# Kernel optimization log

Hardware: AMD Instinct MI355X
Metric: run time of the kernel (lower is better)

The kernel has to match this reference:

```python
import jax, jax.numpy as jnp
import numpy as np

K, NR, NT, D, NLAYER = 128, 1, 128, 1, 8
PMAX = float(np.power(10.0, 10.0 / 10.0))  # snr=10 dB
SIGMA = 1.0


def _cx(x):
    # [2, ...] real/imag-stacked -> complex
    return x[0] + 1j * x[1]


def _ct(x):
    # conjugate transpose on last two axes
    return jnp.conj(jnp.swapaxes(x, -1, -2))


def _layer(Vc, Hc, up1, up3, up4, wp1, wp3, vp1, vp2, vp4):
    # Vc: [K,Nt,d] complex, Hc: [K,Nr,Nt] complex; params complex, batched over K.
    cdt = Vc.dtype
    I_nr = jnp.eye(NR, dtype=cdt)
    I_d = jnp.eye(D, dtype=cdt)
    I_nt = jnp.eye(NT, dtype=cdt)
    # ---- A_update: A_i = sigma/Pmax * sum_j tr(V_j V_j^H) * I + H_i (sum_j V_j V_j^H) H_i^H
    tr_vv = jnp.einsum('knd,knd->', Vc, jnp.conj(Vc))          # complex scalar
    S = jnp.einsum('knd,kmd->nm', Vc, jnp.conj(Vc))            # [Nt,Nt]
    A = (SIGMA / PMAX) * tr_vv * I_nr + jnp.einsum('krt,tm,ksm->krs', Hc, S, jnp.conj(Hc))  # [K,Nr,Nr]
    # ---- U layer: A_inv_i = p1_i inv(A_i) + 0.01 p3_i ; U_i = A_inv_i H_i V_i + p4_i
    A_inv = up1 @ jnp.linalg.inv(A) + 0.01 * up3
    Un = A_inv @ Hc @ Vc + up4                                  # [K,Nr,d]
    # ---- E_update: E_i = I - U_i^H H_i V_i
    E = I_d - _ct(Un) @ Hc @ Vc                                 # [K,d,d]
    # ---- W layer: W_i = 0.1 p1_i inv(E_i) + 0.01 p3_i
    Wn = 0.1 * (wp1 @ jnp.linalg.inv(E)) + 0.01 * wp3           # [K,d,d]
    # ---- B_update: B = sigma/Pmax * sum_i tr(U_i W_i U_i^H) * I + sum_i H_i^H U_i W_i U_i^H H_i (same for all users)
    UWU = Un @ Wn @ _ct(Un)                                     # [K,Nr,Nr]
    tr_uwu = jnp.trace(UWU, axis1=-2, axis2=-1).sum()
    B = (SIGMA / PMAX) * tr_uwu * I_nt + jnp.sum(_ct(Hc) @ UWU @ Hc, axis=0)  # [Nt,Nt]
    B_inv = jnp.linalg.inv(B)
    # ---- V
    if vp2 is None:  # FinalV: V_i = inv(B) H_i^H U_i W_i
        Vn = (B_inv @ _ct(Hc)) @ Un @ Wn
    else:            # V layer: B_inv_i = p2_i inv(B) + 0.01 p4_i ; V_i = B_inv_i H_i^H U_i W_i + p1_i
        Bm = vp2 @ B_inv + 0.01 * vp4
        Vn = Bm @ _ct(Hc) @ Un @ Wn + vp1
    # ---- Normalize: scale by sqrt(Pmax)/sqrt(Re sum_j tr(V_j V_j^H))
    pw = jnp.sqrt(jnp.real(jnp.einsum('knd,knd->', Vn, jnp.conj(Vn))))
    return (jnp.sqrt(PMAX) / pw) * Vn


def setup_inputs() -> dict:
    key = jax.random.key(0)
    ks = jax.random.split(key, 20)
    f32 = jnp.float32
    def rn(k, shape, scale):
        return (scale * jax.random.normal(k, shape)).astype(f32)
    inp = {
        'V': rn(ks[0], (2, K, NT, D), 1.0),
        'H': rn(ks[1], (2, K, NR, NT), 1.0),
        # mid-layer params, stacked over layers: only params actually used in forward
        'mid_u_p1': rn(ks[2], (NLAYER, 2, K, NR, NR), 0.001),
        'mid_u_p3': rn(ks[3], (NLAYER, 2, K, NR, NR), 0.01),
        'mid_u_p4': rn(ks[4], (NLAYER, 2, K, NR, D), 0.01),
        'mid_w_p1': rn(ks[5], (NLAYER, 2, K, D, D), 0.001),
        'mid_w_p3': rn(ks[6], (NLAYER, 2, K, D, D), 0.01),
        'mid_v_p1': rn(ks[7], (NLAYER, 2, K, NT, D), 0.001),
        'mid_v_p2': rn(ks[8], (NLAYER, 2, K, NT, NT), 0.01),
        'mid_v_p4': rn(ks[9], (NLAYER, 2, K, NT, NT), 0.01),
        # final layer (U + W only)
        'fin_u_p1': rn(ks[10], (2, K, NR, NR), 0.001),
        'fin_u_p3': rn(ks[11], (2, K, NR, NR), 0.01),
        'fin_u_p4': rn(ks[12], (2, K, NR, D), 0.01),
        'fin_w_p1': rn(ks[13], (2, K, D, D), 0.001),
        'fin_w_p3': rn(ks[14], (2, K, D, D), 0.01),
    }
    return inp


def reference(V, H, mid_u_p1, mid_u_p3, mid_u_p4, mid_w_p1, mid_w_p3,
              mid_v_p1, mid_v_p2, mid_v_p4,
              fin_u_p1, fin_u_p3, fin_u_p4, fin_w_p1, fin_w_p3):
    Vc = _cx(V)
    Hc = _cx(H)
    n = mid_u_p1.shape[0]
    for l in range(n):
        Vc = _layer(Vc, Hc,
                    _cx(mid_u_p1[l]), _cx(mid_u_p3[l]), _cx(mid_u_p4[l]),
                    _cx(mid_w_p1[l]), _cx(mid_w_p3[l]),
                    _cx(mid_v_p1[l]), _cx(mid_v_p2[l]), _cx(mid_v_p4[l]))
    Vc = _layer(Vc, Hc,
                _cx(fin_u_p1), _cx(fin_u_p3), _cx(fin_u_p4),
                _cx(fin_w_p1), _cx(fin_w_p3), None, None, None)
    return jnp.stack([jnp.real(Vc), jnp.imag(Vc)]).astype(jnp.float32)
```

## Files before the change

### kernel.cpp

```cpp
#include <hip/hip_runtime.h>
#include <math.h>

#define KK 128
#define NTT 128
#define PMAXF 10.0f
#define SP 0.1f
#define LUT 512
#define LDA2 130

typedef float2 c32;

__device__ __forceinline__ c32 cmul(c32 a, c32 b){
    return make_float2(a.x*b.x - a.y*b.y, a.x*b.y + a.y*b.x);
}
__device__ __forceinline__ c32 cmulc(c32 a, c32 b){
    return make_float2(a.x*b.x + a.y*b.y, a.y*b.x - a.x*b.y);
}
__device__ __forceinline__ c32 cinv(c32 a){
    float d = 1.0f/(a.x*a.x + a.y*a.y);
    return make_float2(a.x*d, -a.y*d);
}

__global__ void k_trvv(const float* __restrict__ V0, float* __restrict__ out){
    float s = 0.f;
    for (int e = blockIdx.x*blockDim.x + threadIdx.x; e < 2*KK*NTT; e += gridDim.x*blockDim.x){
        float v = V0[e]; s += v*v;
    }
    __shared__ float red[4];
    for (int d = 32; d; d >>= 1) s += __shfl_down(s, d);
    int lane = threadIdx.x & 63, w = threadIdx.x >> 6;
    if (!lane) red[w] = s;
    __syncthreads();
    if (!threadIdx.x){
        float t = red[0] + red[1] + red[2] + red[3];
        atomicAdd(out, t);
    }
}

__global__ void k_stage1(const float* __restrict__ Hre, const float* __restrict__ Him,
                         const float* __restrict__ V0re, const float* __restrict__ V0im,
                         const float2* __restrict__ VN, int use_vn,
                         const float* __restrict__ pw2prev,
                         const float* __restrict__ trvvp,
                         const float* __restrict__ u1, const float* __restrict__ u3,
                         const float* __restrict__ u4, const float* __restrict__ w1,
                         const float* __restrict__ w3,
                         float* __restrict__ wre, float* __restrict__ wim,
                         float* __restrict__ sre, float* __restrict__ sim,
                         float* __restrict__ sumw)
{
    int k = blockIdx.x, j = threadIdx.x;
    __shared__ float hre_s[NTT], him_s[NTT];
    __shared__ float redq[NTT];
    __shared__ c32 pkk_s;
    hre_s[j] = Hre[k*NTT + j];
    him_s[j] = Him[k*NTT + j];
    __syncthreads();

    float g = 1.0f;
    if (pw2prev) g = sqrtf(PMAXF / *pw2prev);

    float pre = 0.f, pim = 0.f;
    if (use_vn){
        const float2* vr = VN + j*NTT;
        #pragma unroll 4
        for (int n = 0; n < NTT; n++){
            float2 v = vr[n];
            pre += hre_s[n]*v.x - him_s[n]*v.y;
            pim += hre_s[n]*v.y + him_s[n]*v.x;
        }
    } else {
        const float* vr = V0re + j*NTT;
        const float* vi = V0im + j*NTT;
        #pragma unroll 4
        for (int n = 0; n < NTT; n++){
            float a = vr[n], b = vi[n];
            pre += hre_s[n]*a - him_s[n]*b;
            pim += hre_s[n]*b + him_s[n]*a;
        }
    }
    pre *= g; pim *= g;
    if (j == k) pkk_s = make_float2(pre, pim);
    redq[j] = pre*pre + pim*pim;
    __syncthreads();
    for (int d = 64; d; d >>= 1){
        if (j < d) redq[j] += redq[j + d];
        __syncthreads();
    }
    if (j == 0){
        float trvv = pw2prev ? PMAXF : *trvvp;
        float A = SP*trvv + redq[0];
        float invA = 1.0f/A;
        c32 p1 = make_float2(u1[k], u1[KK + k]);
        c32 p3 = make_float2(u3[k], u3[KK + k]);
        c32 p4 = make_float2(u4[k], u4[KK + k]);
        c32 Ainv = make_float2(p1.x*invA + 0.01f*p3.x, p1.y*invA + 0.01f*p3.y);
        c32 Pkk = pkk_s;
        c32 U = cmul(Ainv, Pkk); U.x += p4.x; U.y += p4.y;
        c32 t = cmulc(Pkk, U);
        c32 E = make_float2(1.0f - t.x, -t.y);
        c32 iE = cinv(E);
        c32 q1 = make_float2(w1[k], w1[KK + k]);
        c32 q3 = make_float2(w3[k], w3[KK + k]);
        c32 W = cmul(q1, iE);
        W.x = 0.1f*W.x + 0.01f*q3.x;
        W.y = 0.1f*W.y + 0.01f*q3.y;
        float u2 = U.x*U.x + U.y*U.y;
        c32 wk = make_float2(u2*W.x, u2*W.y);
        c32 sk = cmul(U, W);
        wre[k] = wk.x; wim[k] = wk.y;
        sre[k] = sk.x; sim[k] = sk.y;
        atomicAdd(&sumw[0], wk.x);
        atomicAdd(&sumw[1], wk.y);
    }
}

__global__ void k_bbuild(const float* __restrict__ Hre, const float* __restrict__ Him,
                         const float* __restrict__ wre, const float* __restrict__ wim,
                         const float* __restrict__ sumw, float2* __restrict__ B)
{
    int n = blockIdx.x, m = threadIdx.x;
    __shared__ float cr[KK], ci[KK];
    {
        int k = m;
        c32 h = make_float2(Hre[k*NTT + n], -Him[k*NTT + n]);
        c32 wk = make_float2(wre[k], wim[k]);
        c32 t = cmul(h, wk);
        cr[k] = t.x; ci[k] = t.y;
    }
    __syncthreads();
    float br = 0.f, bi = 0.f;
    #pragma unroll 4
    for (int k = 0; k < KK; k++){
        float hr = Hre[k*NTT + m], hi = Him[k*NTT + m];
        br += cr[k]*hr - ci[k]*hi;
        bi += cr[k]*hi + ci[k]*hr;
    }
    if (n == m){ br += SP*sumw[0]; bi += SP*sumw[1]; }
    B[n*NTT + m] = make_float2(br, bi);
}

__global__ void __launch_bounds__(512, 1) k_lu7(const float2* __restrict__ B,
                                                float2* __restrict__ BT,
                                                float2* __restrict__ rcg,
                                                int* __restrict__ permg)
{
    extern __shared__ float2 As[];
    __shared__ float2 rc_s[KK];
    __shared__ float2 Msc[112*16];
    const int t = threadIdx.x;

    {
        const float4* B4 = (const float4*)B;
        float4* A4 = (float4*)As;
        for (int e = t; e < KK*64; e += LUT){
            int r = e >> 6, cq = e & 63;
            A4[r*65 + cq] = B4[e];
        }
    }
    __syncthreads();

    for (int j = 0; j < 8; ++j){
        const int J0 = j*16, T0 = J0 + 16, Rt = 128 - T0;

        for (int ii = 0; ii < 16; ++ii){
            const int gi = J0 + ii;
            float2 piv = As[gi*LDA2 + gi];
            float2 rc = cinv(piv);
            if (t == 0) rc_s[gi] = rc;
            const int W1 = 15 - ii;
            if (W1 > 0){
                {
                    int ci = t & 15, ti0 = t >> 4;
                    if (ci < W1){
                        int c = gi + 1 + ci;
                        for (int rr = gi + 1 + ti0; rr < 128; rr += 32){
                            float2 m = cmul(As[rr*LDA2 + gi], rc);
                            float2 u = As[gi*LDA2 + c];
                            float2 a = As[rr*LDA2 + c];
                            a.x -= m.x*u.x - m.y*u.y;
                            a.y -= m.x*u.y + m.y*u.x;
                            As[rr*LDA2 + c] = a;
                        }
                    }
                }
                if (Rt > 0){
                    int ri = t & 15, cj0 = t >> 4;
                    if (ri < W1){
                        int rr = gi + 1 + ri;
                        float2 m = cmul(As[rr*LDA2 + gi], rc);
                        for (int c = T0 + cj0; c < 128; c += 32){
                            float2 u = As[gi*LDA2 + c];
                            float2 a = As[rr*LDA2 + c];
                            a.x -= m.x*u.x - m.y*u.y;
                            a.y -= m.x*u.y + m.y*u.x;
                            As[rr*LDA2 + c] = a;
                        }
                    }
                }
            }
            __syncthreads();
        }
        if (j == 7) break;

        for (int e = t; e < Rt*16; e += LUT){
            int rp = e >> 4, i = e & 15;
            Msc[e] = cmul(As[(T0 + rp)*LDA2 + J0 + i], rc_s[J0 + i]);
        }
        __syncthreads();

        {
            int cl = t & 63, g = t >> 6;
            if (2*cl < Rt){
                int c0 = T0 + 2*cl;
                float4 u2[16];
                #pragma unroll
                for (int i = 0; i < 16; ++i)
                    u2[i] = *(const float4*)&As[(J0 + i)*LDA2 + c0];
                int rows = Rt >> 3;
                int rbeg = T0 + g*rows;
                for (int r = rbeg; r < rbeg + rows; ++r){
                    int rp = r - T0;
                    float4 a = *(const float4*)&As[r*LDA2 + c0];
                    #pragma unroll
                    for (int i = 0; i < 16; ++i){
                        float2 m = Msc[rp*16 + i];
                        float4 u = u2[i];
                        a.x -= m.x*u.x - m.y*u.y;
                        a.y -= m.x*u.y + m.y*u.x;
                        a.z -= m.x*u.z - m.y*u.w;
                        a.w -= m.x*u.w + m.y*u.z;
                    }
                    *(float4*)&As[r*LDA2 + c0] = a;
                }
            }
        }
        __syncthreads();
    }

    for (int e = t; e < KK*NTT; e += LUT){
        int c = e >> 7, r = e & 127;
        BT[e] = As[r*LDA2 + c];
    }
    if (t < KK){ rcg[t] = rc_s[t]; permg[t] = t; }
}

__global__ void k_solve(const float2* __restrict__ BT, const float2* __restrict__ rcg,
                        const int* __restrict__ permg,
                        const float* __restrict__ Hre, const float* __restrict__ Him,
                        float2* __restrict__ X)
{
    int c = blockIdx.x;
    int lane = threadIdx.x;
    __shared__ float2 rc_s[KK];
    rc_s[lane] = rcg[lane];
    rc_s[lane + 64] = rcg[lane + 64];
    int r0 = lane, r1 = lane + 64;
    int o0 = permg[r0], o1 = permg[r1];
    float2 b0 = make_float2(Hre[c*NTT + o0], -Him[c*NTT + o0]);
    float2 b1 = make_float2(Hre[c*NTT + o1], -Him[c*NTT + o1]);
    __syncthreads();

    float2 cur0[8], cur1[8];
    #pragma unroll
    for (int jj = 0; jj < 8; jj++){ cur0[jj] = BT[jj*NTT + r0]; cur1[jj] = BT[jj*NTT + r1]; }
    for (int ib = 0; ib < 16; ib++){
        float2 n0[8], n1[8];
        if (ib < 15){
            int nb = (ib + 1)*8;
            #pragma unroll
            for (int jj = 0; jj < 8; jj++){ n0[jj] = BT[(nb + jj)*NTT + r0]; n1[jj] = BT[(nb + jj)*NTT + r1]; }
        }
        #pragma unroll
        for (int jj = 0; jj < 8; jj++){
            int i = ib*8 + jj;
            float xr, xi;
            if (i < 64){ xr = __shfl(b0.x, i);      xi = __shfl(b0.y, i); }
            else       { xr = __shfl(b1.x, i - 64); xi = __shfl(b1.y, i - 64); }
            float2 rc = rc_s[i];
            float tr = rc.x*xr - rc.y*xi, ti = rc.x*xi + rc.y*xr;
            float2 l0 = cur0[jj], l1 = cur1[jj];
            if (r0 > i){ b0.x -= l0.x*tr - l0.y*ti; b0.y -= l0.x*ti + l0.y*tr; }
            if (r1 > i){ b1.x -= l1.x*tr - l1.y*ti; b1.y -= l1.x*ti + l1.y*tr; }
        }
        if (ib < 15){
            #pragma unroll
            for (int jj = 0; jj < 8; jj++){ cur0[jj] = n0[jj]; cur1[jj] = n1[jj]; }
        }
    }
    #pragma unroll
    for (int jj = 0; jj < 8; jj++){ cur0[jj] = BT[(120 + jj)*NTT + r0]; cur1[jj] = BT[(120 + jj)*NTT + r1]; }
    for (int ib = 15; ib >= 0; ib--){
        float2 n0[8], n1[8];
        if (ib > 0){
            int nb = (ib - 1)*8;
            #pragma unroll
            for (int jj = 0; jj < 8; jj++){ n0[jj] = BT[(nb + jj)*NTT + r0]; n1[jj] = BT[(nb + jj)*NTT + r1]; }
        }
        #pragma unroll
        for (int jj = 7; jj >= 0; jj--){
            int i = ib*8 + jj;
            float yr, yi;
            if (i < 64){ yr = __shfl(b0.x, i);      yi = __shfl(b0.y, i); }
            else       { yr = __shfl(b1.x, i - 64); yi = __shfl(b1.y, i - 64); }
            float2 rc = rc_s[i];
            float xr = rc.x*yr - rc.y*yi, xi = rc.x*yi + rc.y*yr;
            if (r0 == i){ b0.x = xr; b0.y = xi; }
            if (r1 == i){ b1.x = xr; b1.y = xi; }
            float2 u0 = cur0[jj], u1v = cur1[jj];
            if (r0 < i){ b0.x -= u0.x*xr - u0.y*xi; b0.y -= u0.x*xi + u0.y*xr; }
            if (r1 < i){ b1.x -= u1v.x*xr - u1v.y*xi; b1.y -= u1v.x*xi + u1v.y*xr; }
        }
        if (ib > 0){
            #pragma unroll
            for (int jj = 0; jj < 8; jj++){ cur0[jj] = n0[jj]; cur1[jj] = n1[jj]; }
        }
    }
    X[c*NTT + r0] = b0;
    X[c*NTT + r1] = b1;
}

__global__ void __launch_bounds__(512) k_mvz(const float* __restrict__ p2re, const float* __restrict__ p2im,
                                             const float* __restrict__ p4re, const float* __restrict__ p4im,
                                             const float2* __restrict__ X,
                                             const float* __restrict__ Hre, const float* __restrict__ Him,
                                             const float* __restrict__ sre, const float* __restrict__ sim,
                                             const float* __restrict__ p1re, const float* __restrict__ p1im,
                                             float2* __restrict__ VN, float* __restrict__ pw2)
{
    int b = blockIdx.x;
    int k = b >> 1, rh = b & 1;
    int t = threadIdx.x;
    __shared__ float2 xv[NTT], hv[NTT];
    __shared__ float red[8];
    if (t < NTT){
        xv[t] = X[k*NTT + t];
        hv[t] = make_float2(Hre[k*NTT + t], -Him[k*NTT + t]);
    }
    __syncthreads();
    int rl = t >> 3, j = t & 7;
    int row = rh*64 + rl;
    size_t base = (size_t)k*16384 + (size_t)row*128 + (size_t)j*16;
    const float* a2r = p2re + base;
    const float* a2i = p2im + base;
    const float* a4r = p4re + base;
    const float* a4i = p4im + base;
    float yr = 0.f, yi = 0.f, zr = 0.f, zi = 0.f;
    #pragma unroll
    for (int ii = 0; ii < 4; ++ii){
        float4 ar = *(const float4*)(a2r + 4*ii);
        float4 ai = *(const float4*)(a2i + 4*ii);
        float4 br = *(const float4*)(a4r + 4*ii);
        float4 bi = *(const float4*)(a4i + 4*ii);
        float2 x0 = xv[j*16 + 4*ii],     x1 = xv[j*16 + 4*ii + 1];
        float2 x2 = xv[j*16 + 4*ii + 2], x3 = xv[j*16 + 4*ii + 3];
        float2 h0 = hv[j*16 + 4*ii],     h1 = hv[j*16 + 4*ii + 1];
        float2 h2 = hv[j*16 + 4*ii + 2], h3 = hv[j*16 + 4*ii + 3];
        yr += ar.x*x0.x - ai.x*x0.y;  yi += ar.x*x0.y + ai.x*x0.x;
        yr += ar.y*x1.x - ai.y*x1.y;  yi += ar.y*x1.y + ai.y*x1.x;
        yr += ar.z*x2.x - ai.z*x2.y;  yi += ar.z*x2.y + ai.z*x2.x;
        yr += ar.w*x3.x - ai.w*x3.y;  yi += ar.w*x3.y + ai.w*x3.x;
        zr += br.x*h0.x - bi.x*h0.y;  zi += br.x*h0.y + bi.x*h0.x;
        zr += br.y*h1.x - bi.y*h1.y;  zi += br.y*h1.y + bi.y*h1.x;
        zr += br.z*h2.x - bi.z*h2.y;  zi += br.z*h2.y + bi.z*h2.x;
        zr += br.w*h3.x - bi.w*h3.y;  zi += br.w*h3.y + bi.w*h3.x;
    }
    #pragma unroll
    for (int d = 1; d < 8; d <<= 1){
        yr += __shfl_xor(yr, d); yi += __shfl_xor(yi, d);
        zr += __shfl_xor(zr, d); zi += __shfl_xor(zi, d);
    }
    float pwl = 0.f;
    if (j == 0){
        c32 s = make_float2(sre[k], sim[k]);
        float2 y = make_float2(yr + 0.01f*zr, yi + 0.01f*zi);
        c32 v = cmul(s, y);
        v.x += p1re[k*NTT + row]; v.y += p1im[k*NTT + row];
        VN[k*NTT + row] = v;
        pwl = v.x*v.x + v.y*v.y;
    }
    for (int d = 32; d; d >>= 1) pwl += __shfl_down(pwl, d);
    int lane = t & 63, w = t >> 6;
    if (!lane) red[w] = pwl;
    __syncthreads();
    if (!t){
        float tt = 0.f;
        #pragma unroll
        for (int w2 = 0; w2 < 8; ++w2) tt += red[w2];
        atomicAdd(pw2, tt);
    }
}

__global__ void k_finout(const float2* __restrict__ X,
                         const float* __restrict__ sre, const float* __restrict__ sim,
                         float2* __restrict__ VN, float* __restrict__ pw2)
{
    float acc = 0.f;
    for (int e = blockIdx.x*blockDim.x + threadIdx.x; e < KK*NTT; e += gridDim.x*blockDim.x){
        int k = e >> 7;
        c32 s = make_float2(sre[k], sim[k]);
        c32 v = cmul(s, X[e]);
        VN[e] = v;
        acc += v.x*v.x + v.y*v.y;
    }
    __shared__ float red[4];
    for (int d = 32; d; d >>= 1) acc += __shfl_down(acc, d);
    int lane = threadIdx.x & 63, w = threadIdx.x >> 6;
    if (!lane) red[w] = acc;
    __syncthreads();
    if (!threadIdx.x) atomicAdd(pw2, red[0] + red[1] + red[2] + red[3]);
}

__global__ void k_write(const float2* __restrict__ VN, const float* __restrict__ pw2,
                        float* __restrict__ out)
{
    float gsc = sqrtf(PMAXF / *pw2);
    for (int e = blockIdx.x*blockDim.x + threadIdx.x; e < KK*NTT; e += gridDim.x*blockDim.x){
        float2 v = VN[e];
        out[e] = gsc*v.x;
        out[KK*NTT + e] = gsc*v.y;
    }
}

extern "C" void kernel_launch(void* const* d_in, const int* in_sizes, int n_in,
                              void* d_out, int out_size, void* d_ws, size_t ws_size,
                              hipStream_t stream)
{
    const float* V0  = (const float*)d_in[0];
    const float* H   = (const float*)d_in[1];
    const float* mu1 = (const float*)d_in[2];
    const float* mu3 = (const float*)d_in[3];
    const float* mu4 = (const float*)d_in[4];
    const float* mw1 = (const float*)d_in[5];
    const float* mw3 = (const float*)d_in[6];
    const float* mv1 = (const float*)d_in[7];
    const float* mv2 = (const float*)d_in[8];
    const float* mv4 = (const float*)d_in[9];
    const float* fu1 = (const float*)d_in[10];
    const float* fu3 = (const float*)d_in[11];
    const float* fu4 = (const float*)d_in[12];
    const float* fw1 = (const float*)d_in[13];
    const float* fw3 = (const float*)d_in[14];

    float* ws = (float*)d_ws;
    float*  acc  = ws;
    float*  wre  = ws + 64;
    float*  wim  = ws + 192;
    float*  sre  = ws + 320;
    float*  sim  = ws + 448;
    float2* B    = (float2*)(ws + 1024);
    float2* rc   = (float2*)(ws + 33792);
    int*    perm = (int*)  (ws + 34048);
    float2* X    = (float2*)(ws + 34176);
    float2* VN   = (float2*)(ws + 132480);
    float2* BT   = (float2*)(ws + 165248);

    const int LU_LDS = KK*LDA2*sizeof(float2);
    (void)hipFuncSetAttribute((const void*)k_lu7,
                              hipFuncAttributeMaxDynamicSharedMemorySize, LU_LDS);

    hipMemsetAsync(ws, 0, 64*sizeof(float), stream);
    k_trvv<<<64, 256, 0, stream>>>(V0, ws + 40);

    const float* Hre = H;
    const float* Him = H + 16384;

    for (int l = 0; l < 9; l++){
        bool fin = (l == 8);
        const float* u1 = fin ? fu1 : mu1 + (size_t)l*256;
        const float* u3 = fin ? fu3 : mu3 + (size_t)l*256;
        const float* u4 = fin ? fu4 : mu4 + (size_t)l*256;
        const float* w1 = fin ? fw1 : mw1 + (size_t)l*256;
        const float* w3 = fin ? fw3 : mw3 + (size_t)l*256;

        k_stage1<<<128, 128, 0, stream>>>(Hre, Him, V0, V0 + 16384, VN, (l > 0) ? 1 : 0,
                                          (l > 0) ? (acc + (l - 1)*4 + 2) : nullptr,
                                          ws + 40,
                                          u1, u3, u4, w1, w3,
                                          wre, wim, sre, sim, acc + l*4);
        k_bbuild<<<128, 128, 0, stream>>>(Hre, Him, wre, wim, acc + l*4, B);
        k_lu7<<<1, 512, LU_LDS, stream>>>(B, BT, rc, perm);
        k_solve<<<128, 64, 0, stream>>>(BT, rc, perm, Hre, Him, X);

        if (!fin){
            const float* p2 = mv2 + (size_t)l*4194304;
            const float* p4 = mv4 + (size_t)l*4194304;
            const float* p1 = mv1 + (size_t)l*32768;
            k_mvz<<<256, 512, 0, stream>>>(p2, p2 + 2097152, p4, p4 + 2097152,
                                           X, Hre, Him, sre, sim,
                                           p1, p1 + 16384, VN, acc + l*4 + 2);
        } else {
            k_finout<<<64, 256, 0, stream>>>(X, sre, sim, VN, acc + l*4 + 2);
            k_write<<<64, 256, 0, stream>>>(VN, acc + l*4 + 2, (float*)d_out);
        }
    }
}
```

Baseline: 1.903 ms.

## Keep LU panel columns in registers and factor panel with one sync per pivot

The single-block blocked LU on the 128x128 complex matrix now holds each row's 16-column panel in registers. Each pivot step broadcasts the pivot row through a small shared buffer, so the panel factorization works mostly in registers with one barrier per pivot. The U-block triangular solve is done separately per column, and the trailing update processes two rows per iteration using a transposed multiplier buffer. Results are written to BT directly as each panel finishes, replacing the final transpose pass. This targets the serial latency and barrier count of the LU kernel, which runs on one workgroup per layer, at the cost of more register pressure and more complex indexing.

```diff
diff --git a/kernel.cpp b/kernel.cpp
--- a/kernel.cpp
+++ b/kernel.cpp
@@ -5,7 +5,6 @@
 #define NTT 128
 #define PMAXF 10.0f
 #define SP 0.1f
-#define LUT 512
 #define LDA2 130
 
 typedef float2 c32;
@@ -140,20 +139,22 @@
     B[n*NTT + m] = make_float2(br, bi);
 }
 
-__global__ void __launch_bounds__(512, 1) k_lu7(const float2* __restrict__ B,
+__global__ void __launch_bounds__(512, 1) k_lu8(const float2* __restrict__ B,
                                                 float2* __restrict__ BT,
                                                 float2* __restrict__ rcg,
                                                 int* __restrict__ permg)
 {
     extern __shared__ float2 As[];
+    __shared__ float2 Prow[2][16];
+    __shared__ float2 Mpan[16*17];
+    __shared__ float2 MscT[16*114];
     __shared__ float2 rc_s[KK];
-    __shared__ float2 Msc[112*16];
     const int t = threadIdx.x;
 
     {
         const float4* B4 = (const float4*)B;
         float4* A4 = (float4*)As;
-        for (int e = t; e < KK*64; e += LUT){
+        for (int e = t; e < KK*64; e += 512){
             int r = e >> 6, cq = e & 63;
             A4[r*65 + cq] = B4[e];
         }
@@ -162,50 +163,82 @@
 
     for (int j = 0; j < 8; ++j){
         const int J0 = j*16, T0 = J0 + 16, Rt = 128 - T0;
-
+        const bool inrow = (t < 128) && (t >= J0);
+
+        float2 a[16];
+        if (inrow){
+            #pragma unroll
+            for (int h = 0; h < 8; ++h){
+                float4 q = *(const float4*)&As[t*LDA2 + J0 + 2*h];
+                a[2*h]   = make_float2(q.x, q.y);
+                a[2*h+1] = make_float2(q.z, q.w);
+            }
+        }
+
+        #pragma unroll 1
         for (int ii = 0; ii < 16; ++ii){
-            const int gi = J0 + ii;
-            float2 piv = As[gi*LDA2 + gi];
+            if (t == J0 + ii){
+                #pragma unroll
+                for (int c = 0; c < 16; ++c) Prow[ii & 1][c] = a[c];
+            }
+            __syncthreads();
+            float2 piv = Prow[ii & 1][ii];
             float2 rc = cinv(piv);
-            if (t == 0) rc_s[gi] = rc;
-            const int W1 = 15 - ii;
-            if (W1 > 0){
-                {
-                    int ci = t & 15, ti0 = t >> 4;
-                    if (ci < W1){
-                        int c = gi + 1 + ci;
-                        for (int rr = gi + 1 + ti0; rr < 128; rr += 32){
-                            float2 m = cmul(As[rr*LDA2 + gi], rc);
-                            float2 u = As[gi*LDA2 + c];
-                            float2 a = As[rr*LDA2 + c];
-                            a.x -= m.x*u.x - m.y*u.y;
-                            a.y -= m.x*u.y + m.y*u.x;
-                            As[rr*LDA2 + c] = a;
-                        }
-                    }
-                }
-                if (Rt > 0){
-                    int ri = t & 15, cj0 = t >> 4;
-                    if (ri < W1){
-                        int rr = gi + 1 + ri;
-                        float2 m = cmul(As[rr*LDA2 + gi], rc);
-                        for (int c = T0 + cj0; c < 128; c += 32){
-                            float2 u = As[gi*LDA2 + c];
-                            float2 a = As[rr*LDA2 + c];
-                            a.x -= m.x*u.x - m.y*u.y;
-                            a.y -= m.x*u.y + m.y*u.x;
-                            As[rr*LDA2 + c] = a;
-                        }
+            if (t == 0) rc_s[J0 + ii] = rc;
+            if (inrow && t > J0 + ii){
+                float2 m = cmul(a[ii], rc);
+                #pragma unroll
+                for (int c = 0; c < 16; ++c){
+                    if (c > ii){
+                        float2 u = Prow[ii & 1][c];
+                        a[c].x -= m.x*u.x - m.y*u.y;
+                        a[c].y -= m.x*u.y + m.y*u.x;
                     }
                 }
             }
-            __syncthreads();
+        }
+        __syncthreads();
+
+        if (inrow){
+            #pragma unroll
+            for (int c = 0; c < 16; ++c)
+                BT[(J0 + c)*KK + t] = a[c];
         }
         if (j == 7) break;
 
-        for (int e = t; e < Rt*16; e += LUT){
-            int rp = e >> 4, i = e & 15;
-            Msc[e] = cmul(As[(T0 + rp)*LDA2 + J0 + i], rc_s[J0 + i]);
+        if (t > J0 && t < T0){
+            int p = t - J0;
+            #pragma unroll
+            for (int i = 0; i < 16; ++i) Mpan[p*17 + i] = a[i];
+        }
+        if (t >= T0 && t < 128){
+            int rp = t - T0;
+            #pragma unroll
+            for (int i = 0; i < 16; ++i)
+                MscT[i*114 + rp] = cmul(a[i], rc_s[J0 + i]);
+        }
+        __syncthreads();
+
+        if (t < Rt){
+            int c = T0 + t;
+            float2 u[16];
+            #pragma unroll
+            for (int i = 0; i < 16; ++i) u[i] = As[(J0 + i)*LDA2 + c];
+            #pragma unroll
+            for (int a2 = 1; a2 < 16; ++a2){
+                #pragma unroll
+                for (int i = 0; i < 16; ++i){
+                    if (i < a2){
+                        float2 mm = cmul(Mpan[a2*17 + i], rc_s[J0 + i]);
+                        u[a2].x -= mm.x*u[i].x - mm.y*u[i].y;
+                        u[a2].y -= mm.x*u[i].y + mm.y*u[i].x;
+                    }
+                }
+            }
+            #pragma unroll
+            for (int a2 = 1; a2 < 16; ++a2) As[(J0 + a2)*LDA2 + c] = u[a2];
+            #pragma unroll
+            for (int a2 = 0; a2 < 16; ++a2) BT[c*KK + (J0 + a2)] = u[a2];
         }
         __syncthreads();
 
@@ -217,31 +250,28 @@
                 #pragma unroll
                 for (int i = 0; i < 16; ++i)
                     u2[i] = *(const float4*)&As[(J0 + i)*LDA2 + c0];
-                int rows = Rt >> 3;
-                int rbeg = T0 + g*rows;
-                for (int r = rbeg; r < rbeg + rows; ++r){
-                    int rp = r - T0;
-                    float4 a = *(const float4*)&As[r*LDA2 + c0];
+                int nb = Rt >> 1;
+                for (int rb = g; rb < nb; rb += 8){
+                    int r0 = T0 + 2*rb;
+                    float4 a0 = *(const float4*)&As[r0*LDA2 + c0];
+                    float4 a1 = *(const float4*)&As[(r0 + 1)*LDA2 + c0];
                     #pragma unroll
                     for (int i = 0; i < 16; ++i){
-                        float2 m = Msc[rp*16 + i];
+                        float4 mm = *(const float4*)&MscT[i*114 + 2*rb];
                         float4 u = u2[i];
-                        a.x -= m.x*u.x - m.y*u.y;
-                        a.y -= m.x*u.y + m.y*u.x;
-                        a.z -= m.x*u.z - m.y*u.w;
-                        a.w -= m.x*u.w + m.y*u.z;
+                        a0.x -= mm.x*u.x - mm.y*u.y;  a0.y -= mm.x*u.y + mm.y*u.x;
+                        a0.z -= mm.x*u.z - mm.y*u.w;  a0.w -= mm.x*u.w + mm.y*u.z;
+                        a1.x -= mm.z*u.x - mm.w*u.y;  a1.y -= mm.z*u.y + mm.w*u.x;
+                        a1.z -= mm.z*u.z - mm.w*u.w;  a1.w -= mm.z*u.w + mm.w*u.z;
                     }
-                    *(float4*)&As[r*LDA2 + c0] = a;
+                    *(float4*)&As[r0*LDA2 + c0] = a0;
+                    *(float4*)&As[(r0 + 1)*LDA2 + c0] = a1;
                 }
             }
         }
         __syncthreads();
     }
 
-    for (int e = t; e < KK*NTT; e += LUT){
-        int c = e >> 7, r = e & 127;
-        BT[e] = As[r*LDA2 + c];
-    }
     if (t < KK){ rcg[t] = rc_s[t]; permg[t] = t; }
 }
 
@@ -456,7 +486,7 @@
     float2* BT   = (float2*)(ws + 165248);
 
     const int LU_LDS = KK*LDA2*sizeof(float2);
-    (void)hipFuncSetAttribute((const void*)k_lu7,
+    (void)hipFuncSetAttribute((const void*)k_lu8,
                               hipFuncAttributeMaxDynamicSharedMemorySize, LU_LDS);
 
     hipMemsetAsync(ws, 0, 64*sizeof(float), stream);
@@ -479,7 +509,7 @@
                                           u1, u3, u4, w1, w3,
                                           wre, wim, sre, sim, acc + l*4);
         k_bbuild<<<128, 128, 0, stream>>>(Hre, Him, wre, wim, acc + l*4, B);
-        k_lu7<<<1, 512, LU_LDS, stream>>>(B, BT, rc, perm);
+        k_lu8<<<1, 512, LU_LDS, stream>>>(B, BT, rc, perm);
         k_solve<<<128, 64, 0, stream>>>(BT, rc, perm, Hre, Him, X);
 
         if (!fin){
```

Result: slower. 2.965 ms (+55.8%).
